# Kernel tuning notes

Measured on AMD Instinct MI355X. Metric: run time of the kernel, lower is better.

## Reference

```python
import jax, jax.numpy as jnp
import numpy as np

B, L, HID, H, FF = 32, 1024, 512, 8, 2048
DH = HID // H  # head_dim = 64; deterministic FAVOR features => M == DH
KEPS = 1e-3    # performer kernel_epsilon
LN_EPS = 1e-6  # flax LayerNorm default


def setup_inputs() -> dict:
    key = jax.random.key(0)
    ks = jax.random.split(key, 12)
    sa = 1.0 / np.sqrt(HID)
    sf = 1.0 / np.sqrt(FF)
    return {
        "x": jax.random.normal(ks[0], (B, L, HID), jnp.float32),
        "Wq": jax.random.normal(ks[1], (HID, H, DH), jnp.float32) * sa,
        "bq": jnp.zeros((H, DH), jnp.float32),
        "Wk": jax.random.normal(ks[2], (HID, H, DH), jnp.float32) * sa,
        "bk": jnp.zeros((H, DH), jnp.float32),
        "Wv": jax.random.normal(ks[3], (HID, H, DH), jnp.float32) * sa,
        "bv": jnp.zeros((H, DH), jnp.float32),
        "Wo": jax.random.normal(ks[4], (H, DH, HID), jnp.float32) * sa,
        "bo": jnp.zeros((HID,), jnp.float32),
        "ln1_scale": jnp.ones((HID,), jnp.float32),
        "ln1_bias": jnp.zeros((HID,), jnp.float32),
        "W1": jax.random.normal(ks[5], (HID, FF), jnp.float32) * sa,
        "b1": jnp.zeros((FF,), jnp.float32),
        "W2": jax.random.normal(ks[6], (FF, HID), jnp.float32) * sf,
        "b2": jnp.zeros((HID,), jnp.float32),
        "ln2_scale": jnp.ones((HID,), jnp.float32),
        "ln2_bias": jnp.zeros((HID,), jnp.float32),
    }


def _layernorm(x, scale, bias):
    mu = jnp.mean(x, axis=-1, keepdims=True)
    var = jnp.mean(jnp.square(x - mu), axis=-1, keepdims=True)
    return (x - mu) * jax.lax.rsqrt(var + LN_EPS) * scale + bias


def _favor_bidirectional(q, k, v):
    # Performer generalized attention, deterministic features:
    # phi(x) = relu(x) + kernel_epsilon, renormalized.
    qp = jax.nn.relu(q) + KEPS  # [B,L,H,M]
    kp = jax.nn.relu(k) + KEPS  # [B,L,H,M]
    kv = jnp.einsum('blhm,blhd->bhmd', kp, v)        # [B,H,M,D]
    num = jnp.einsum('blhm,bhmd->blhd', qp, kv)      # [B,L,H,D]
    den = jnp.einsum('blhm,bhm->blh', qp, kp.sum(axis=1))  # [B,L,H]
    return num / den[..., None]


def reference(x, Wq, bq, Wk, bk, Wv, bv, Wo, bo,
              ln1_scale, ln1_bias, W1, b1, W2, b2, ln2_scale, ln2_bias):
    # Multi-head projections (flax MHA DenseGeneral layout [HID,H,DH])
    q = jnp.einsum('blc,chd->blhd', x, Wq) + bq
    k = jnp.einsum('blc,chd->blhd', x, Wk) + bk
    v = jnp.einsum('blc,chd->blhd', x, Wv) + bv
    attn = _favor_bidirectional(q, k, v)                  # [B,L,H,DH]
    attended = jnp.einsum('blhd,hdc->blc', attn, Wo) + bo # [B,L,HID]
    h = _layernorm(attended + x, ln1_scale, ln1_bias)
    ff = jax.nn.relu(h @ W1 + b1) @ W2 + b2
    return _layernorm(ff + h, ln2_scale, ln2_bias)
```

## Files before the change

### kernel.cpp

```cpp
#include <hip/hip_runtime.h>


#define DI __device__ __forceinline__
#define AS1 __attribute__((address_space(1)))
#define AS3 __attribute__((address_space(3)))
#define GLD16(g, l) __builtin_amdgcn_global_load_lds((const AS1 void*)(g), (AS3 void*)(l), 16, 0, 0)

typedef __attribute__((ext_vector_type(8))) short bf16x8;
typedef __attribute__((ext_vector_type(4))) float f32x4;

DI float b2f(short s){ unsigned int u = ((unsigned int)(unsigned short)s) << 16; float f; __builtin_memcpy(&f, &u, 4); return f; }
DI short f2b(float f){ unsigned int u; __builtin_memcpy(&u, &f, 4); u += 0x7fffu + ((u >> 16) & 1u); return (short)(u >> 16); }

constexpr int Ll = 1024;
constexpr int SPLIT = 16384;

__global__ __launch_bounds__(256) void k_cvt_x(const float* __restrict__ x, short* __restrict__ xb){
  long i = (long)blockIdx.x * 256 + threadIdx.x;
  const float4* p = (const float4*)x + i * 2;
  float4 a = p[0], b = p[1];
  bf16x8 o;
  o[0]=f2b(a.x); o[1]=f2b(a.y); o[2]=f2b(a.z); o[3]=f2b(a.w);
  o[4]=f2b(b.x); o[5]=f2b(b.y); o[6]=f2b(b.z); o[7]=f2b(b.w);
  *((bf16x8*)xb + i) = o;
}

__global__ void k_tcvt(const float* __restrict__ in, short* __restrict__ out, int R, int C){
  __shared__ float t[32][33];
  int c0 = blockIdx.x * 32, r0 = blockIdx.y * 32;
  int x = threadIdx.x, y = threadIdx.y;
  #pragma unroll
  for (int j = 0; j < 4; ++j) t[y + 8*j][x] = in[(long)(r0 + y + 8*j) * C + c0 + x];
  __syncthreads();
  #pragma unroll
  for (int j = 0; j < 4; ++j) out[(long)(c0 + y + 8*j) * R + r0 + x] = f2b(t[x][y + 8*j]);
}

__global__ void k_tcvt4(const float* __restrict__ s0, const float* __restrict__ s1,
                        const float* __restrict__ s2, const float* __restrict__ s3,
                        short* __restrict__ d0, short* __restrict__ d1,
                        short* __restrict__ d2, short* __restrict__ d3){
  __shared__ float t[32][33];
  int z = blockIdx.z;
  const float* in = z == 0 ? s0 : z == 1 ? s1 : z == 2 ? s2 : s3;
  short* out      = z == 0 ? d0 : z == 1 ? d1 : z == 2 ? d2 : d3;
  int c0 = blockIdx.x * 32, r0 = blockIdx.y * 32;
  int x = threadIdx.x, y = threadIdx.y;
  #pragma unroll
  for (int j = 0; j < 4; ++j) t[y + 8*j][x] = in[(long)(r0 + y + 8*j) * 512 + c0 + x];
  __syncthreads();
  #pragma unroll
  for (int j = 0; j < 4; ++j) out[(long)(c0 + y + 8*j) * 512 + r0 + x] = f2b(t[x][y + 8*j]);
}

__global__ void k_pack_bias(const float* __restrict__ bq, const float* __restrict__ bk,
                            const float* __restrict__ bv, float* __restrict__ bqkv){
  int i = blockIdx.x * 256 + threadIdx.x;
  if (i < 512) bqkv[i] = bq[i];
  else if (i < 1024) bqkv[i] = bk[i - 512];
  else if (i < 1536) bqkv[i] = bv[i - 1024];
}

template<int EPI, int KD>
__global__ __launch_bounds__(512, 2) void k_gemm256(
    const short* __restrict__ A0, const short* __restrict__ A1,
    const short* __restrict__ BT, int NT,
    const float* __restrict__ bias, const short* __restrict__ residX,
    short* __restrict__ oQ, short* __restrict__ oK, short* __restrict__ oV,
    short* __restrict__ o1)
{
  __shared__ short lds[65536];
  const int tid = threadIdx.x;
  const int w = tid >> 6, lane = tid & 63;
  const int wm = w >> 2, wn = w & 3;
  const int lg = lane >> 4, lr = lane & 15;
  const int lrow = lane >> 3, lslot = (lane & 7) ^ lrow;

  const int per = gridDim.x >> 3;
  const int wg = (blockIdx.x & 7) * per + (blockIdx.x >> 3);
  const long m0 = (long)(wg / NT) * 256, n0 = (long)(wg % NT) * 256;

  const short* Ause = A0;
  long mbase = m0;
  if (A1 != A0 && m0 >= SPLIT) { Ause = A1; mbase = m0 - SPLIT; }

  f32x4 acc[8][4];
  #pragma unroll
  for (int i = 0; i < 8; ++i)
    #pragma unroll
    for (int j = 0; j < 4; ++j) acc[i][j] = 0.f;

  const char* Abase = (const char*)lds + wm * 16384;
  const char* Bbase = (const char*)lds + 65536 + (wn >> 1) * 16384;

#define STAGE_A(buf, half, t) do {                                              \
    int k0_ = (t) * 64;                                                         \
    _Pragma("unroll")                                                           \
    for (int q_ = 0; q_ < 2; ++q_) {                                            \
      int rs_ = w * 16 + q_ * 8;                                                \
      GLD16(Ause + (mbase + (half) * 128 + rs_ + lrow) * KD + k0_ + lslot * 8,  \
            (char*)lds + ((buf) * 16384 + (half) * 8192 + rs_ * 64) * 2);       \
    } } while (0)
#define STAGE_B(buf, half, t) do {                                              \
    int k0_ = (t) * 64;                                                         \
    _Pragma("unroll")                                                           \
    for (int q_ = 0; q_ < 2; ++q_) {                                            \
      int rs_ = w * 16 + q_ * 8;                                                \
      GLD16(BT + (n0 + (half) * 128 + rs_ + lrow) * KD + k0_ + lslot * 8,       \
            (char*)lds + (32768 + (buf) * 16384 + (half) * 8192 + rs_ * 64) * 2); \
    } } while (0)
#define READ_A(buf, qr) do {                                                    \
    _Pragma("unroll")                                                           \
    for (int i_ = 0; i_ < 4; ++i_)                                              \
      _Pragma("unroll")                                                         \
      for (int kk_ = 0; kk_ < 2; ++kk_) {                                       \
        int ra_ = (qr) * 64 + i_ * 16 + lr;                                     \
        fA[i_][kk_] = *(const bf16x8*)(Abase + (buf) * 32768 + ra_ * 128 +      \
                       ((kk_ * 64 + lg * 16) ^ ((ra_ & 7) << 4)));              \
      } } while (0)
#define READ_B(FB, buf, qc) do {                                                \
    _Pragma("unroll")                                                           \
    for (int j_ = 0; j_ < 2; ++j_)                                              \
      _Pragma("unroll")                                                         \
      for (int kk_ = 0; kk_ < 2; ++kk_) {                                       \
        int rb_ = (wn & 1) * 64 + (qc) * 32 + j_ * 16 + lr;                     \
        FB[j_][kk_] = *(const bf16x8*)(Bbase + (buf) * 32768 + rb_ * 128 +      \
                       ((kk_ * 64 + lg * 16) ^ ((rb_ & 7) << 4)));              \
      } } while (0)
#define MFMA_Q(qr, qc, FB) do {                                                 \
    __builtin_amdgcn_s_setprio(1);                                              \
    _Pragma("unroll")                                                           \
    for (int i_ = 0; i_ < 4; ++i_)                                              \
      _Pragma("unroll")                                                         \
      for (int j_ = 0; j_ < 2; ++j_)                                            \
        _Pragma("unroll")                                                       \
        for (int kk_ = 0; kk_ < 2; ++kk_)                                       \
          acc[(qr)*4+i_][(qc)*2+j_] = __builtin_amdgcn_mfma_f32_16x16x32_bf16(  \
              fA[i_][kk_], FB[j_][kk_], acc[(qr)*4+i_][(qc)*2+j_], 0, 0, 0);    \
    __builtin_amdgcn_s_setprio(0);                                              \
  } while (0)
#define BARR __builtin_amdgcn_s_barrier()
#define GATEC asm volatile("s_waitcnt vmcnt(4)" ::: "memory")
#define GATE0 asm volatile("s_waitcnt vmcnt(0)" ::: "memory")

  constexpr int NKT = KD / 64;
  bf16x8 fA[4][2], fB0[2][2], fB1[2][2];

  STAGE_A(0, 0, 0); STAGE_A(0, 1, 0); STAGE_B(0, 0, 0); STAGE_B(0, 1, 0);
  STAGE_B(1, 0, 1); STAGE_B(1, 1, 1);
  GATEC; BARR;

  for (int it = 0; it < NKT / 2; ++it) {
    const int t0 = 2 * it, t1 = 2 * it + 1;
    const bool s0 = (t0 + 2 < NKT), s1 = (t1 + 2 < NKT);
    READ_A(0, 0); READ_B(fB0, 0, 0); STAGE_A(1, 0, t1);
    BARR; MFMA_Q(0, 0, fB0); BARR;
    READ_B(fB1, 0, 1); STAGE_A(1, 1, t1);
    BARR; MFMA_Q(0, 1, fB1); BARR;
    READ_A(0, 1); if (s0) STAGE_B(0, 0, t0 + 2);
    BARR; MFMA_Q(1, 0, fB0); BARR;
    if (s0) { STAGE_B(0, 1, t0 + 2); GATEC; } else { GATE0; }
    BARR; MFMA_Q(1, 1, fB1); BARR;
    READ_A(1, 0); READ_B(fB0, 1, 0); if (s0) STAGE_A(0, 0, t0 + 2);
    BARR; MFMA_Q(0, 0, fB0); BARR;
    READ_B(fB1, 1, 1); if (s0) STAGE_A(0, 1, t0 + 2);
    BARR; MFMA_Q(0, 1, fB1); BARR;
    READ_A(1, 1); if (s1) STAGE_B(1, 0, t1 + 2);
    BARR; MFMA_Q(1, 0, fB0); BARR;
    if (s1) { STAGE_B(1, 1, t1 + 2); GATEC; } else { GATE0; }
    BARR; MFMA_Q(1, 1, fB1); BARR;
  }

#undef STAGE_A
#undef STAGE_B
#undef READ_A
#undef READ_B
#undef MFMA_Q
#undef BARR
#undef GATEC
#undef GATE0

  #pragma unroll
  for (int fr = 0; fr < 8; ++fr)
    #pragma unroll
    for (int fc = 0; fc < 4; ++fc)
      #pragma unroll
      for (int r = 0; r < 4; ++r) {
        int grow = (int)m0 + wm * 128 + fr * 16 + lg * 4 + r;
        int gcol = (int)n0 + wn * 64 + fc * 16 + lr;
        float v = acc[fr][fc][r];
        if constexpr (EPI == 0) {
          v += bias[gcol];
          int which = gcol >> 9, hd = gcol & 511, h = hd >> 6, d = hd & 63;
          int b = grow >> 10, l = grow & 1023;
          long o = ((long)(b * 8 + h) * 1024 + l) * 64 + d;
          if (which == 2) oV[o] = f2b(v);
          else { float p = fmaxf(v, 0.f) + 1e-3f; if (which) oK[o] = f2b(p); else oQ[o] = f2b(p); }
        } else if constexpr (EPI == 1) {
          v += bias[gcol] + b2f(residX[(long)grow * 512 + gcol]);
          oQ[(long)grow * 512 + gcol] = f2b(v);
        } else if constexpr (EPI == 2) {
          v = fmaxf(v + bias[gcol], 0.f);
          if (grow < SPLIT) oQ[(long)grow * 2048 + gcol] = f2b(v);
          else              o1[(long)(grow - SPLIT) * 2048 + gcol] = f2b(v);
        } else {
          long idx = (long)grow * 512 + gcol;
          v += bias[gcol] + b2f(oQ[idx]);
          oQ[idx] = f2b(v);
        }
      }
}

__global__ __launch_bounds__(256) void k_fkv_part(const short* __restrict__ kp, const short* __restrict__ vb,
                                                  float* __restrict__ kvp, float* __restrict__ ksp)
{
  constexpr int LS = 72;
  __shared__ short kps[64 * LS];
  __shared__ short vps[64 * LS];
  int bh = blockIdx.x & 255, c = blockIdx.x >> 8;
  const short* kpp = kp + (long)bh * Ll * 64;
  const short* vpp = vb + (long)bh * Ll * 64;
  int tid = threadIdx.x;
  int mb = (tid & 15) * 4, db = (tid >> 4) * 4;
  float acc[4][4];
  float ks[4] = {0.f, 0.f, 0.f, 0.f};
  #pragma unroll
  for (int i = 0; i < 4; ++i)
    #pragma unroll
    for (int j = 0; j < 4; ++j) acc[i][j] = 0.f;

  for (int l0 = c * 256; l0 < c * 256 + 256; l0 += 64) {
    __syncthreads();
    #pragma unroll
    for (int s = 0; s < 2; ++s) {
      int idx = tid + s * 256;
      int row = idx >> 3, c8 = idx & 7;
      *(bf16x8*)(&kps[row * LS + c8 * 8]) = *(const bf16x8*)(kpp + (long)(l0 + row) * 64 + c8 * 8);
      *(bf16x8*)(&vps[row * LS + c8 * 8]) = *(const bf16x8*)(vpp + (long)(l0 + row) * 64 + c8 * 8);
    }
    __syncthreads();
    #pragma unroll 4
    for (int l = 0; l < 64; ++l) {
      short4 ka = *(const short4*)(&kps[l * LS + mb]);
      short4 va = *(const short4*)(&vps[l * LS + db]);
      float kf[4] = {b2f(ka.x), b2f(ka.y), b2f(ka.z), b2f(ka.w)};
      float vf[4] = {b2f(va.x), b2f(va.y), b2f(va.z), b2f(va.w)};
      if (tid < 16) { ks[0] += kf[0]; ks[1] += kf[1]; ks[2] += kf[2]; ks[3] += kf[3]; }
      #pragma unroll
      for (int i = 0; i < 4; ++i)
        #pragma unroll
        for (int j = 0; j < 4; ++j) acc[i][j] += kf[i] * vf[j];
    }
  }
  float* kout = kvp + (long)c * 1048576 + (long)bh * 4096;
  #pragma unroll
  for (int i = 0; i < 4; ++i)
    #pragma unroll
    for (int j = 0; j < 4; ++j)
      kout[(db + j) * 64 + mb + i] = acc[i][j];
  if (tid < 16) {
    #pragma unroll
    for (int i = 0; i < 4; ++i) ksp[(long)c * 16384 + bh * 64 + mb + i] = ks[i];
  }
}

__global__ __launch_bounds__(256) void k_fkv_reduce(const float* __restrict__ kvp, const float* __restrict__ ksp,
                                                    short* __restrict__ kvt, float* __restrict__ ksum)
{
  int g = blockIdx.x * 256 + threadIdx.x;
  float s = kvp[g] + kvp[g + 1048576] + kvp[g + 2 * 1048576] + kvp[g + 3 * 1048576];
  kvt[g] = f2b(s);
  if (g < 16384)
    ksum[g] = ksp[g] + ksp[g + 16384] + ksp[g + 2 * 16384] + ksp[g + 3 * 16384];
}

__global__ __launch_bounds__(256) void k_favor_num(const short* __restrict__ qp, const short* __restrict__ kvt,
                                                   const float* __restrict__ ksum, short* __restrict__ attn)
{
  constexpr int LS = 72;
  __shared__ short Qs[128 * 64];
  __shared__ short kvs[64 * LS];
  __shared__ float part[256];
  __shared__ float den[128];
  int bh = blockIdx.x >> 3, lt = blockIdx.x & 7;
  int b = bh >> 3, h = bh & 7;
  const short* qpp = qp + ((long)bh * Ll + lt * 128) * 64;
  int tid = threadIdx.x;
  int wave = tid >> 6, lane = tid & 63;
  int lrow = lane >> 3, lslot = (lane & 7) ^ lrow;

  #pragma unroll
  for (int s = 0; s < 4; ++s) {
    int rs = (s * 4 + wave) * 8;
    GLD16(qpp + (long)(rs + lrow) * 64 + lslot * 8, &Qs[rs * 64]);
  }
  #pragma unroll
  for (int s = 0; s < 2; ++s) {
    int idx = tid + s * 256;
    int row = idx >> 3, c8 = idx & 7;
    *(bf16x8*)(&kvs[row * LS + c8 * 8]) = *(const bf16x8*)(kvt + (long)bh * 4096 + row * 64 + c8 * 8);
  }
  __syncthreads();
  {
    int r = tid >> 1, half = tid & 1;
    const float* kss = ksum + bh * 64 + half * 32;
    float s = 0.f;
    #pragma unroll
    for (int c = 0; c < 4; ++c) {
      int cc = half * 4 + c;
      bf16x8 v = *(const bf16x8*)((const char*)Qs + r * 128 + ((cc * 16) ^ ((r & 7) << 4)));
      #pragma unroll
      for (int j = 0; j < 8; ++j) s += b2f(v[j]) * kss[c * 8 + j];
    }
    part[tid] = s;
  }
  __syncthreads();
  if (tid < 128) den[tid] = part[2 * tid] + part[2 * tid + 1];
  __syncthreads();

  int wr = wave >> 1, wc = wave & 1;
  int lg = lane >> 4, lr = lane & 15;
  f32x4 acc[4][2];
  #pragma unroll
  for (int i = 0; i < 4; ++i) { acc[i][0] = 0.f; acc[i][1] = 0.f; }
  #pragma unroll
  for (int kk = 0; kk < 2; ++kk) {
    bf16x8 af[4], bfr[2];
    #pragma unroll
    for (int i = 0; i < 4; ++i) {
      int ra = wr * 64 + i * 16 + lr;
      af[i] = *(const bf16x8*)((const char*)Qs + ra * 128 + ((kk * 64 + lg * 16) ^ ((ra & 7) << 4)));
    }
    #pragma unroll
    for (int j = 0; j < 2; ++j)
      bfr[j] = *(const bf16x8*)(&kvs[(wc * 32 + j * 16 + lr) * LS + kk * 32 + lg * 8]);
    #pragma unroll
    for (int i = 0; i < 4; ++i)
      #pragma unroll
      for (int j = 0; j < 2; ++j)
        acc[i][j] = __builtin_amdgcn_mfma_f32_16x16x32_bf16(af[i], bfr[j], acc[i][j], 0, 0, 0);
  }
  #pragma unroll
  for (int i = 0; i < 4; ++i)
    #pragma unroll
    for (int j = 0; j < 2; ++j)
      #pragma unroll
      for (int r = 0; r < 4; ++r) {
        int rl = wr * 64 + i * 16 + lg * 4 + r;
        int d  = wc * 32 + j * 16 + lr;
        int t  = b * Ll + lt * 128 + rl;
        attn[(long)t * 512 + h * 64 + d] = f2b(acc[i][j][r] / den[rl]);
      }
}

__global__ __launch_bounds__(256) void k_ln_bb(const short* __restrict__ in, const float* __restrict__ sc,
                                               const float* __restrict__ bi, short* __restrict__ ob)
{
  int row = blockIdx.x * 4 + (threadIdx.x >> 6);
  int lane = threadIdx.x & 63;
  bf16x8 v = *((const bf16x8*)(in + (long)row * 512) + lane);
  float e[8];
  #pragma unroll
  for (int j = 0; j < 8; ++j) e[j] = b2f(v[j]);
  float s = 0.f, s2 = 0.f;
  #pragma unroll
  for (int j = 0; j < 8; ++j) { s += e[j]; s2 += e[j] * e[j]; }
  #pragma unroll
  for (int off = 32; off; off >>= 1) { s += __shfl_xor(s, off); s2 += __shfl_xor(s2, off); }
  float mu = s * (1.f / 512.f);
  float var = s2 * (1.f / 512.f) - mu * mu;
  float rstd = rsqrtf(var + 1e-6f);
  int c0 = lane * 8;
  bf16x8 o;
  #pragma unroll
  for (int j = 0; j < 8; ++j) o[j] = f2b((e[j] - mu) * rstd * sc[c0 + j] + bi[c0 + j]);
  *((bf16x8*)(ob + (long)row * 512) + lane) = o;
}

__global__ __launch_bounds__(256) void k_ln_bf(const short* __restrict__ in, const float* __restrict__ sc,
                                               const float* __restrict__ bi, float* __restrict__ of)
{
  int row = blockIdx.x * 4 + (threadIdx.x >> 6);
  int lane = threadIdx.x & 63;
  bf16x8 v = *((const bf16x8*)(in + (long)row * 512) + lane);
  float e[8];
  #pragma unroll
  for (int j = 0; j < 8; ++j) e[j] = b2f(v[j]);
  float s = 0.f, s2 = 0.f;
  #pragma unroll
  for (int j = 0; j < 8; ++j) { s += e[j]; s2 += e[j] * e[j]; }
  #pragma unroll
  for (int off = 32; off; off >>= 1) { s += __shfl_xor(s, off); s2 += __shfl_xor(s2, off); }
  float mu = s * (1.f / 512.f);
  float var = s2 * (1.f / 512.f) - mu * mu;
  float rstd = rsqrtf(var + 1e-6f);
  int c0 = lane * 8;
  float o0[4], o1[4];
  #pragma unroll
  for (int j = 0; j < 4; ++j) {
    o0[j] = (e[j]     - mu) * rstd * sc[c0 + j]     + bi[c0 + j];
    o1[j] = (e[4 + j] - mu) * rstd * sc[c0 + 4 + j] + bi[c0 + 4 + j];
  }
  *(float4*)(of + (long)row * 512 + c0)     = (float4){o0[0], o0[1], o0[2], o0[3]};
  *(float4*)(of + (long)row * 512 + c0 + 4) = (float4){o1[0], o1[1], o1[2], o1[3]};
}

extern "C" void kernel_launch(void* const* d_in, const int* in_sizes, int n_in,
                              void* d_out, int out_size, void* d_ws, size_t ws_size,
                              hipStream_t stream)
{
  const float* x   = (const float*)d_in[0];
  const float* Wq  = (const float*)d_in[1];
  const float* bq  = (const float*)d_in[2];
  const float* Wk  = (const float*)d_in[3];
  const float* bk  = (const float*)d_in[4];
  const float* Wv  = (const float*)d_in[5];
  const float* bv  = (const float*)d_in[6];
  const float* Wo  = (const float*)d_in[7];
  const float* bo  = (const float*)d_in[8];
  const float* g1  = (const float*)d_in[9];
  const float* be1 = (const float*)d_in[10];
  const float* W1  = (const float*)d_in[11];
  const float* b1  = (const float*)d_in[12];
  const float* W2  = (const float*)d_in[13];
  const float* b2  = (const float*)d_in[14];
  const float* g2  = (const float*)d_in[15];
  const float* be2 = (const float*)d_in[16];
  float* out = (float*)d_out;

  const long MB = 1024L * 1024L;
  char* ws = (char*)d_ws;
  short* qp    = (short*)(ws + 0 * MB);
  short* kp    = (short*)(ws + 32 * MB);
  short* vb    = (short*)(ws + 64 * MB);
  short* attn  = (short*)(ws + 32 * MB);
  short* hb    = (short*)(ws + 0 * MB);
  short* hpreB = (short*)(ws + 64 * MB);
  short* ffa0  = (short*)(ws + 32 * MB);
  short* wqkvT = (short*)(ws + 96 * MB);
  short* woT   = (short*)(ws + 98 * MB);
  short* w1T   = (short*)(ws + 99 * MB);
  short* w2T   = (short*)(ws + 101 * MB);
  short* kvt   = (short*)(ws + 103 * MB);
  float* ksum  = (float*)(ws + 105 * MB);
  float* bqkv  = (float*)(ws + 105 * MB + 65536);

  short* xb   = (short*)d_out;
  float* kvp  = (float*)((char*)d_out + 32 * MB);
  float* ksp  = (float*)((char*)d_out + 48 * MB);
  short* ffa1 = (short*)d_out;

  dim3 tb(32, 8);
  k_cvt_x<<<8192, 256, 0, stream>>>(x, xb);
  k_tcvt4<<<dim3(16, 16, 4), tb, 0, stream>>>(Wq, Wk, Wv, Wo,
      wqkvT, wqkvT + 512 * 512, wqkvT + 1024 * 512, woT);
  k_tcvt<<<dim3(64, 16), tb, 0, stream>>>(W1, w1T, 512, 2048);
  k_tcvt<<<dim3(16, 64), tb, 0, stream>>>(W2, w2T, 2048, 512);
  k_pack_bias<<<6, 256, 0, stream>>>(bq, bk, bv, bqkv);

  k_gemm256<0, 512><<<768, 512, 0, stream>>>(xb, xb, wqkvT, 6, bqkv, nullptr, qp, kp, vb, nullptr);
  k_fkv_part<<<1024, 256, 0, stream>>>(kp, vb, kvp, ksp);
  k_fkv_reduce<<<4096, 256, 0, stream>>>(kvp, ksp, kvt, ksum);
  k_favor_num<<<2048, 256, 0, stream>>>(qp, kvt, ksum, attn);
  k_gemm256<1, 512><<<256, 512, 0, stream>>>(attn, attn, woT, 2, bo, xb, hpreB, nullptr, nullptr, nullptr);
  k_ln_bb<<<8192, 256, 0, stream>>>(hpreB, g1, be1, hb);
  k_gemm256<2, 512><<<1024, 512, 0, stream>>>(hb, hb, w1T, 8, b1, nullptr, ffa0, nullptr, nullptr, ffa1);
  k_gemm256<3, 2048><<<256, 512, 0, stream>>>(ffa0, ffa1, w2T, 2, b2, nullptr, hb, nullptr, nullptr, nullptr);
  k_ln_bf<<<8192, 256, 0, stream>>>(hb, g2, be2, out);
}
```

Measured before the change: 365.8 us.

## Merge prep kernels into one launch and add sched barriers in GEMM loop

Folds the x conversion, the four weight transpose-convert kernels and the bias pack into a single k_prep launch that branches on block index, cutting four kernel launches and the gaps between them. Separately, it puts compiler scheduling barriers after each staging/read group in the GEMM main loop so the compiler cannot move LDS reads and global-to-LDS loads across the MFMA phases. The merged kernel still runs a __syncthreads on the transpose path only, which is uniform per block. The scheduling barriers may also stop the compiler from interleaving useful work.

```diff
diff --git a/kernel.cpp b/kernel.cpp
--- a/kernel.cpp
+++ b/kernel.cpp
@@ -15,47 +15,52 @@
 constexpr int Ll = 1024;
 constexpr int SPLIT = 16384;
 
-__global__ __launch_bounds__(256) void k_cvt_x(const float* __restrict__ x, short* __restrict__ xb){
-  long i = (long)blockIdx.x * 256 + threadIdx.x;
-  const float4* p = (const float4*)x + i * 2;
-  float4 a = p[0], b = p[1];
-  bf16x8 o;
-  o[0]=f2b(a.x); o[1]=f2b(a.y); o[2]=f2b(a.z); o[3]=f2b(a.w);
-  o[4]=f2b(b.x); o[5]=f2b(b.y); o[6]=f2b(b.z); o[7]=f2b(b.w);
-  *((bf16x8*)xb + i) = o;
-}
-
-__global__ void k_tcvt(const float* __restrict__ in, short* __restrict__ out, int R, int C){
-  __shared__ float t[32][33];
-  int c0 = blockIdx.x * 32, r0 = blockIdx.y * 32;
-  int x = threadIdx.x, y = threadIdx.y;
-  #pragma unroll
-  for (int j = 0; j < 4; ++j) t[y + 8*j][x] = in[(long)(r0 + y + 8*j) * C + c0 + x];
-  __syncthreads();
-  #pragma unroll
-  for (int j = 0; j < 4; ++j) out[(long)(c0 + y + 8*j) * R + r0 + x] = f2b(t[x][y + 8*j]);
-}
-
-__global__ void k_tcvt4(const float* __restrict__ s0, const float* __restrict__ s1,
-                        const float* __restrict__ s2, const float* __restrict__ s3,
-                        short* __restrict__ d0, short* __restrict__ d1,
-                        short* __restrict__ d2, short* __restrict__ d3){
-  __shared__ float t[32][33];
-  int z = blockIdx.z;
-  const float* in = z == 0 ? s0 : z == 1 ? s1 : z == 2 ? s2 : s3;
-  short* out      = z == 0 ? d0 : z == 1 ? d1 : z == 2 ? d2 : d3;
-  int c0 = blockIdx.x * 32, r0 = blockIdx.y * 32;
-  int x = threadIdx.x, y = threadIdx.y;
-  #pragma unroll
-  for (int j = 0; j < 4; ++j) t[y + 8*j][x] = in[(long)(r0 + y + 8*j) * 512 + c0 + x];
-  __syncthreads();
-  #pragma unroll
-  for (int j = 0; j < 4; ++j) out[(long)(c0 + y + 8*j) * 512 + r0 + x] = f2b(t[x][y + 8*j]);
-}
-
-__global__ void k_pack_bias(const float* __restrict__ bq, const float* __restrict__ bk,
-                            const float* __restrict__ bv, float* __restrict__ bqkv){
-  int i = blockIdx.x * 256 + threadIdx.x;
+__global__ __launch_bounds__(256) void k_prep(
+    const float* __restrict__ x, short* __restrict__ xb,
+    const float* __restrict__ Wq, const float* __restrict__ Wk,
+    const float* __restrict__ Wv, const float* __restrict__ Wo,
+    short* __restrict__ wqkvT, short* __restrict__ woT,
+    const float* __restrict__ W1, short* __restrict__ w1T,
+    const float* __restrict__ W2, short* __restrict__ w2T,
+    const float* __restrict__ bq, const float* __restrict__ bk,
+    const float* __restrict__ bv, float* __restrict__ bqkv)
+{
+  int bid = blockIdx.x;
+  if (bid < 8192) {
+    long i = (long)bid * 256 + threadIdx.x;
+    const float4* p = (const float4*)x + i * 2;
+    float4 a = p[0], b = p[1];
+    bf16x8 o;
+    o[0]=f2b(a.x); o[1]=f2b(a.y); o[2]=f2b(a.z); o[3]=f2b(a.w);
+    o[4]=f2b(b.x); o[5]=f2b(b.y); o[6]=f2b(b.z); o[7]=f2b(b.w);
+    *((bf16x8*)xb + i) = o;
+    return;
+  }
+  bid -= 8192;
+  if (bid < 3072) {
+    __shared__ float t[32][33];
+    const float* in; short* out; int R, C, bx, by;
+    if (bid < 1024) {
+      int z = bid >> 8, ti = bid & 255;
+      bx = ti & 15; by = ti >> 4; R = 512; C = 512;
+      in  = z == 0 ? Wq : z == 1 ? Wk : z == 2 ? Wv : Wo;
+      out = z == 0 ? wqkvT : z == 1 ? wqkvT + 512 * 512 : z == 2 ? wqkvT + 1024 * 512 : woT;
+    } else if (bid < 2048) {
+      int ti = bid - 1024; bx = ti & 63; by = ti >> 6; R = 512; C = 2048; in = W1; out = w1T;
+    } else {
+      int ti = bid - 2048; bx = ti & 15; by = ti >> 4; R = 2048; C = 512; in = W2; out = w2T;
+    }
+    int c0 = bx * 32, r0 = by * 32;
+    int xx = threadIdx.x & 31, yy = threadIdx.x >> 5;
+    #pragma unroll
+    for (int j = 0; j < 4; ++j) t[yy + 8*j][xx] = in[(long)(r0 + yy + 8*j) * C + c0 + xx];
+    __syncthreads();
+    #pragma unroll
+    for (int j = 0; j < 4; ++j) out[(long)(c0 + yy + 8*j) * R + r0 + xx] = f2b(t[xx][yy + 8*j]);
+    return;
+  }
+  bid -= 3072;
+  int i = bid * 256 + threadIdx.x;
   if (i < 512) bqkv[i] = bq[i];
   else if (i < 1024) bqkv[i] = bk[i - 512];
   else if (i < 1536) bqkv[i] = bv[i - 1024];
@@ -139,6 +144,7 @@
               fA[i_][kk_], FB[j_][kk_], acc[(qr)*4+i_][(qc)*2+j_], 0, 0, 0);    \
     __builtin_amdgcn_s_setprio(0);                                              \
   } while (0)
+#define SPIN __builtin_amdgcn_sched_barrier(0)
 #define BARR __builtin_amdgcn_s_barrier()
 #define GATEC asm volatile("s_waitcnt vmcnt(4)" ::: "memory")
 #define GATE0 asm volatile("s_waitcnt vmcnt(0)" ::: "memory")
@@ -153,21 +159,21 @@
   for (int it = 0; it < NKT / 2; ++it) {
     const int t0 = 2 * it, t1 = 2 * it + 1;
     const bool s0 = (t0 + 2 < NKT), s1 = (t1 + 2 < NKT);
-    READ_A(0, 0); READ_B(fB0, 0, 0); STAGE_A(1, 0, t1);
+    READ_A(0, 0); READ_B(fB0, 0, 0); STAGE_A(1, 0, t1); SPIN;
     BARR; MFMA_Q(0, 0, fB0); BARR;
-    READ_B(fB1, 0, 1); STAGE_A(1, 1, t1);
+    READ_B(fB1, 0, 1); STAGE_A(1, 1, t1); SPIN;
     BARR; MFMA_Q(0, 1, fB1); BARR;
-    READ_A(0, 1); if (s0) STAGE_B(0, 0, t0 + 2);
+    READ_A(0, 1); if (s0) STAGE_B(0, 0, t0 + 2); SPIN;
     BARR; MFMA_Q(1, 0, fB0); BARR;
-    if (s0) { STAGE_B(0, 1, t0 + 2); GATEC; } else { GATE0; }
+    if (s0) { STAGE_B(0, 1, t0 + 2); SPIN; GATEC; } else { SPIN; GATE0; }
     BARR; MFMA_Q(1, 1, fB1); BARR;
-    READ_A(1, 0); READ_B(fB0, 1, 0); if (s0) STAGE_A(0, 0, t0 + 2);
+    READ_A(1, 0); READ_B(fB0, 1, 0); if (s0) STAGE_A(0, 0, t0 + 2); SPIN;
     BARR; MFMA_Q(0, 0, fB0); BARR;
-    READ_B(fB1, 1, 1); if (s0) STAGE_A(0, 1, t0 + 2);
+    READ_B(fB1, 1, 1); if (s0) STAGE_A(0, 1, t0 + 2); SPIN;
     BARR; MFMA_Q(0, 1, fB1); BARR;
-    READ_A(1, 1); if (s1) STAGE_B(1, 0, t1 + 2);
+    READ_A(1, 1); if (s1) STAGE_B(1, 0, t1 + 2); SPIN;
     BARR; MFMA_Q(1, 0, fB0); BARR;
-    if (s1) { STAGE_B(1, 1, t1 + 2); GATEC; } else { GATE0; }
+    if (s1) { STAGE_B(1, 1, t1 + 2); SPIN; GATEC; } else { SPIN; GATE0; }
     BARR; MFMA_Q(1, 1, fB1); BARR;
   }
 
@@ -176,6 +182,7 @@
 #undef READ_A
 #undef READ_B
 #undef MFMA_Q
+#undef SPIN
 #undef BARR
 #undef GATEC
 #undef GATE0
@@ -450,13 +457,8 @@
   float* ksp  = (float*)((char*)d_out + 48 * MB);
   short* ffa1 = (short*)d_out;
 
-  dim3 tb(32, 8);
-  k_cvt_x<<<8192, 256, 0, stream>>>(x, xb);
-  k_tcvt4<<<dim3(16, 16, 4), tb, 0, stream>>>(Wq, Wk, Wv, Wo,
-      wqkvT, wqkvT + 512 * 512, wqkvT + 1024 * 512, woT);
-  k_tcvt<<<dim3(64, 16), tb, 0, stream>>>(W1, w1T, 512, 2048);
-  k_tcvt<<<dim3(16, 64), tb, 0, stream>>>(W2, w2T, 2048, 512);
-  k_pack_bias<<<6, 256, 0, stream>>>(bq, bk, bv, bqkv);
+  k_prep<<<11270, 256, 0, stream>>>(x, xb, Wq, Wk, Wv, Wo, wqkvT, woT,
+                                    W1, w1T, W2, w2T, bq, bk, bv, bqkv);
 
   k_gemm256<0, 512><<<768, 512, 0, stream>>>(xb, xb, wqkvT, 6, bqkv, nullptr, qp, kp, vb, nullptr);
   k_fkv_part<<<1024, 256, 0, stream>>>(kp, vb, kvp, ksp);
```

After: 355.5 us. -2.8%, faster.
